# Kernel tuning notes

Hardware: AMD Instinct MI355X
Metric: run time of the kernel (lower is better)

The kernel has to match this reference:

```python
import jax, jax.numpy as jnp
import numpy as np

FEAT = 1024
ADA = 1024
INTER = 1024
RANK = 8
EPS = 1e-5


def setup_inputs() -> dict:
    key = jax.random.key(0)
    ks = jax.random.split(key, 6)
    B, T = 16, 1024
    x = jax.random.normal(ks[0], (B, T, FEAT), dtype=jnp.float32)
    ada_emb = jax.random.normal(ks[1], (B, ADA), dtype=jnp.float32)
    # learned params (fan-in scaled for numerical sanity)
    W1 = jax.random.normal(ks[2], (ADA, INTER), dtype=jnp.float32) / np.sqrt(ADA)
    b1 = jnp.zeros((INTER,), dtype=jnp.float32)
    W2 = jax.random.normal(ks[3], (INTER, FEAT * RANK * 4), dtype=jnp.float32) * (0.1 / np.sqrt(INTER))
    b2 = jnp.zeros((FEAT * RANK * 4,), dtype=jnp.float32)
    ln_g = jnp.ones((ADA,), dtype=jnp.float32)
    ln_b = jnp.zeros((ADA,), dtype=jnp.float32)
    return {"x": x, "ada_emb": ada_emb, "ln_g": ln_g, "ln_b": ln_b,
            "W1": W1, "b1": b1, "W2": W2, "b2": b2}


def _layernorm(a, g, b):
    mu = jnp.mean(a, axis=-1, keepdims=True)
    var = jnp.mean(jnp.square(a - mu), axis=-1, keepdims=True)
    return (a - mu) * jax.lax.rsqrt(var + EPS) * g + b


def reference(x, ada_emb, ln_g, ln_b, W1, b1, W2, b2):
    B, T, D = x.shape
    # hypernetwork: generate per-sample LoRA factors
    h = jax.nn.gelu(_layernorm(ada_emb, ln_g, ln_b) @ W1 + b1, approximate=False)
    w = h @ W2 + b2                                    # [B, 4*D*rank]
    a1, bb1, a2, bb2 = jnp.split(w, 4, axis=-1)
    a1 = a1.reshape(B, D, RANK)
    bb1 = bb1.reshape(B, D, RANK)
    a2 = a2.reshape(B, D, RANK)
    bb2 = bb2.reshape(B, D, RANK)
    # chained low-rank bmms, broadcast over tokens (== repeat_interleave in torch)
    y = jnp.einsum('btd,bdr->btr', x, a1)
    y = jnp.einsum('btr,bdr->btd', y, bb1)
    y = jax.nn.gelu(y, approximate=False)
    y = jnp.einsum('btd,bdr->btr', y, a2)
    y = jnp.einsum('btr,bdr->btd', y, bb2)
    return y + x
```

## Files before the change

### kernel.cpp

```cpp
#include <hip/hip_runtime.h>
#include <math.h>

typedef unsigned int u32;
typedef unsigned short u16;
typedef unsigned long long u64;

__device__ __forceinline__ u16 f2bf(float f){
  union{float f;u32 u;}v; v.f=f;
  u32 u=v.u; u += 0x7fffu + ((u>>16)&1u);
  return (u16)(u>>16);
}
__device__ __forceinline__ float gelu_exact(float z){
  return 0.5f*z*(1.f + erff(z*0.7071067811865476f));
}
__device__ __forceinline__ void ld8(const uint4* fq, int arr, int d, float* o){
  uint4 v = fq[arr*1024 + d];
  union{u32 i;float f;}c;
  c.i = v.x<<16;        o[0]=c.f;  c.i = v.x&0xffff0000u; o[1]=c.f;
  c.i = v.y<<16;        o[2]=c.f;  c.i = v.y&0xffff0000u; o[3]=c.f;
  c.i = v.z<<16;        o[4]=c.f;  c.i = v.z&0xffff0000u; o[5]=c.f;
  c.i = v.w<<16;        o[6]=c.f;  c.i = v.w&0xffff0000u; o[7]=c.f;
}

__global__ __launch_bounds__(256) void k_hyper1(
    const float* __restrict__ ada, const float* __restrict__ lng, const float* __restrict__ lnb,
    const float* __restrict__ W1, const float* __restrict__ b1, float* __restrict__ hT)
{
  __shared__ float lns[1024];
  __shared__ float red[8];
  __shared__ float cmb[256];
  const int b = blockIdx.y;
  const int tid = threadIdx.x;
  float a4[4]; float s=0.f, s2=0.f;
  #pragma unroll
  for (int i=0;i<4;i++){
    float v = ada[(size_t)b*1024 + tid + 256*i];
    a4[i]=v; s+=v; s2+=v*v;
  }
  #pragma unroll
  for (int m=32;m>=1;m>>=1){ s += __shfl_xor(s,m,64); s2 += __shfl_xor(s2,m,64); }
  if ((tid&63)==0){ red[tid>>6]=s; red[4+(tid>>6)]=s2; }
  __syncthreads();
  s  = red[0]+red[1]+red[2]+red[3];
  s2 = red[4]+red[5]+red[6]+red[7];
  const float mu = s*(1.f/1024.f);
  const float rs = rsqrtf(s2*(1.f/1024.f) - mu*mu + 1e-5f);
  #pragma unroll
  for (int i=0;i<4;i++){
    int k = tid + 256*i;
    lns[k] = (a4[i]-mu)*rs*lng[k] + lnb[k];
  }
  __syncthreads();
  const int c = tid&31;
  const int kq = tid>>5;
  const int col = (blockIdx.x<<5) + c;
  float acc = 0.f;
  #pragma unroll 8
  for (int k=kq*128; k<kq*128+128; k++)
    acc = fmaf(lns[k], W1[(size_t)k*1024 + col], acc);
  cmb[c*8 + kq] = acc;
  __syncthreads();
  if (tid < 32){
    float v = b1[(blockIdx.x<<5) + tid];
    #pragma unroll
    for (int q=0;q<8;q++) v += cmb[tid*8 + q];
    hT[(size_t)((blockIdx.x<<5) + tid)*16 + b] = gelu_exact(v);
  }
}

__global__ __launch_bounds__(256) void k_hyper2(
    const float* __restrict__ hT, const float* __restrict__ W2, const float* __restrict__ b2,
    float* __restrict__ w)
{
  __shared__ float cmb[64*65];
  const int tid = threadIdx.x;
  const int c = tid&63;
  const int kq = tid>>6;
  const int col = (blockIdx.x<<6) + c;
  const float* hbase = hT + (size_t)__builtin_amdgcn_readfirstlane(kq) * 256 * 16;
  float acc[16];
  #pragma unroll
  for (int i=0;i<16;i++) acc[i]=0.f;
  #pragma unroll 4
  for (int k=0;k<256;k++){
    float wv = W2[(size_t)(kq*256 + k)*32768 + col];
    const float* hk = hbase + k*16;
    #pragma unroll
    for (int bb=0;bb<16;bb++) acc[bb] = fmaf(hk[bb], wv, acc[bb]);
  }
  #pragma unroll
  for (int bb=0;bb<16;bb++) cmb[c*65 + kq*16 + bb] = acc[bb];
  __syncthreads();
  if (kq==0){
    float bv = b2[col];
    #pragma unroll
    for (int bb=0;bb<16;bb++)
      w[(size_t)bb*32768 + col] =
        cmb[c*65+bb] + cmb[c*65+16+bb] + cmb[c*65+32+bb] + cmb[c*65+48+bb] + bv;
  }
}

__global__ __launch_bounds__(256, 2) void k_lora(
    const float* __restrict__ x, const float* __restrict__ w, float* __restrict__ out)
{
  __shared__ __align__(16) u16 fsb[4*1024*8];
  const int b = blockIdx.y;
  const int tid = threadIdx.x;
  const float* wb = w + (size_t)b*32768;
  {
    const float4* w4 = (const float4*)wb;
    #pragma unroll 4
    for (int j=0;j<32;j++){
      const int idx4 = tid + 256*j;
      float4 v = w4[idx4];
      union{u16 h[4]; u64 u;} pk;
      pk.h[0]=f2bf(v.x); pk.h[1]=f2bf(v.y);
      pk.h[2]=f2bf(v.z); pk.h[3]=f2bf(v.w);
      *(u64*)&fsb[idx4*4] = pk.u;
    }
  }
  __syncthreads();
  const int l = tid&63;
  const int wv = tid>>6;
  const uint4* fq = (const uint4*)fsb;
  const size_t xbase = (size_t)b*1024*1024;

  #pragma unroll 1
  for (int round=0; round<4; round++){
    const int t0 = blockIdx.x*32 + wv*8 + round*2;
    const float* xr = x + xbase + (size_t)t0*1024 + l;
    float xv0[16], xv1[16];
    #pragma unroll
    for (int i=0;i<16;i++){ xv0[i]=xr[64*i]; xv1[i]=xr[1024+64*i]; }

    float y10[8], y11[8];
    #pragma unroll
    for (int r=0;r<8;r++){ y10[r]=0.f; y11[r]=0.f; }
    #pragma unroll
    for (int i=0;i<16;i++){
      float a[8]; ld8(fq, 0, l+64*i, a);
      #pragma unroll
      for (int r=0;r<8;r++){
        y10[r] = fmaf(xv0[i], a[r], y10[r]);
        y11[r] = fmaf(xv1[i], a[r], y11[r]);
      }
      if ((i&3)==3) __builtin_amdgcn_sched_barrier(0);
    }
    #pragma unroll
    for (int m=32;m>=1;m>>=1){
      #pragma unroll
      for (int r=0;r<8;r++){
        y10[r] += __shfl_xor(y10[r], m, 64);
        y11[r] += __shfl_xor(y11[r], m, 64);
      }
    }

    float y20[8], y21[8];
    #pragma unroll
    for (int r=0;r<8;r++){ y20[r]=0.f; y21[r]=0.f; }
    #pragma unroll
    for (int i=0;i<16;i++){
      float p[8]; ld8(fq, 1, l+64*i, p);
      float z0=0.f, z1=0.f;
      #pragma unroll
      for (int r=0;r<8;r++){ z0=fmaf(y10[r],p[r],z0); z1=fmaf(y11[r],p[r],z1); }
      float g0=gelu_exact(z0), g1=gelu_exact(z1);
      float q[8]; ld8(fq, 2, l+64*i, q);
      #pragma unroll
      for (int r=0;r<8;r++){ y20[r]=fmaf(g0,q[r],y20[r]); y21[r]=fmaf(g1,q[r],y21[r]); }
      if ((i&3)==3) __builtin_amdgcn_sched_barrier(0);
    }
    #pragma unroll
    for (int m=32;m>=1;m>>=1){
      #pragma unroll
      for (int r=0;r<8;r++){
        y20[r] += __shfl_xor(y20[r], m, 64);
        y21[r] += __shfl_xor(y21[r], m, 64);
      }
    }

    #pragma unroll
    for (int i=0;i<16;i++){
      float cc[8]; ld8(fq, 3, l+64*i, cc);
      float o0 = xv0[i], o1 = xv1[i];
      #pragma unroll
      for (int r=0;r<8;r++){
        o0 = fmaf(y20[r], cc[r], o0);
        o1 = fmaf(y21[r], cc[r], o1);
      }
      out[xbase + (size_t)t0*1024 + l + 64*i] = o0;
      out[xbase + (size_t)(t0+1)*1024 + l + 64*i] = o1;
      if ((i&3)==3) __builtin_amdgcn_sched_barrier(0);
    }
  }
}

extern "C" void kernel_launch(void* const* d_in, const int* in_sizes, int n_in,
                              void* d_out, int out_size, void* d_ws, size_t ws_size,
                              hipStream_t stream){
  const float* x    = (const float*)d_in[0];
  const float* ada  = (const float*)d_in[1];
  const float* lng  = (const float*)d_in[2];
  const float* lnb  = (const float*)d_in[3];
  const float* W1   = (const float*)d_in[4];
  const float* b1   = (const float*)d_in[5];
  const float* W2   = (const float*)d_in[6];
  const float* b2   = (const float*)d_in[7];
  float* out = (float*)d_out;
  float* hT  = (float*)d_ws;
  float* w   = (float*)((char*)d_ws + 65536);

  k_hyper1<<<dim3(32,16), 256, 0, stream>>>(ada, lng, lnb, W1, b1, hT);
  k_hyper2<<<dim3(512,1), 256, 0, stream>>>(hT, W2, b2, w);
  k_lora  <<<dim3(32,16), 256, 0, stream>>>(x, w, out);
}
```

Before: 305.0 us.

## Emit bf16 LoRA factors in permuted layout and vectorize x/out access

```diff
diff --git a/kernel.cpp b/kernel.cpp
--- a/kernel.cpp
+++ b/kernel.cpp
@@ -13,8 +13,8 @@
 __device__ __forceinline__ float gelu_exact(float z){
   return 0.5f*z*(1.f + erff(z*0.7071067811865476f));
 }
-__device__ __forceinline__ void ld8(const uint4* fq, int arr, int d, float* o){
-  uint4 v = fq[arr*1024 + d];
+__device__ __forceinline__ void ld8s(const uint4* fq, int slot, float* o){
+  uint4 v = fq[slot];
   union{u32 i;float f;}c;
   c.i = v.x<<16;        o[0]=c.f;  c.i = v.x&0xffff0000u; o[1]=c.f;
   c.i = v.y<<16;        o[2]=c.f;  c.i = v.y&0xffff0000u; o[3]=c.f;
@@ -70,7 +70,7 @@
 
 __global__ __launch_bounds__(256) void k_hyper2(
     const float* __restrict__ hT, const float* __restrict__ W2, const float* __restrict__ b2,
-    float* __restrict__ w)
+    u16* __restrict__ w16)
 {
   __shared__ float cmb[64*65];
   const int tid = threadIdx.x;
@@ -81,7 +81,7 @@
   float acc[16];
   #pragma unroll
   for (int i=0;i<16;i++) acc[i]=0.f;
-  #pragma unroll 4
+  #pragma unroll 8
   for (int k=0;k<256;k++){
     float wv = W2[(size_t)(kq*256 + k)*32768 + col];
     const float* hk = hbase + k*16;
@@ -93,58 +93,63 @@
   __syncthreads();
   if (kq==0){
     float bv = b2[col];
-    #pragma unroll
-    for (int bb=0;bb<16;bb++)
-      w[(size_t)bb*32768 + col] =
-        cmb[c*65+bb] + cmb[c*65+16+bb] + cmb[c*65+32+bb] + cmb[c*65+48+bb] + bv;
+    const int r   = col & 7;
+    const int d   = (col >> 3) & 1023;
+    const int arr = col >> 13;
+    const int slot = (arr<<10) + ((d&3)<<8) + (d>>2);
+    u16* wrec = w16 + ((size_t)slot<<3) + r;
+    #pragma unroll
+    for (int bb=0;bb<16;bb++){
+      float v = cmb[c*65+bb] + cmb[c*65+16+bb] + cmb[c*65+32+bb] + cmb[c*65+48+bb] + bv;
+      wrec[(size_t)bb*32768] = f2bf(v);
+    }
   }
 }
 
 __global__ __launch_bounds__(256, 2) void k_lora(
-    const float* __restrict__ x, const float* __restrict__ w, float* __restrict__ out)
+    const float* __restrict__ x, const u16* __restrict__ w16, float* __restrict__ out)
 {
   __shared__ __align__(16) u16 fsb[4*1024*8];
   const int b = blockIdx.y;
   const int tid = threadIdx.x;
-  const float* wb = w + (size_t)b*32768;
   {
-    const float4* w4 = (const float4*)wb;
+    const uint4* src = (const uint4*)(w16 + (size_t)b*32768);
+    uint4* dst = (uint4*)fsb;
     #pragma unroll 4
-    for (int j=0;j<32;j++){
-      const int idx4 = tid + 256*j;
-      float4 v = w4[idx4];
-      union{u16 h[4]; u64 u;} pk;
-      pk.h[0]=f2bf(v.x); pk.h[1]=f2bf(v.y);
-      pk.h[2]=f2bf(v.z); pk.h[3]=f2bf(v.w);
-      *(u64*)&fsb[idx4*4] = pk.u;
-    }
+    for (int j=0;j<16;j++) dst[tid + 256*j] = src[tid + 256*j];
   }
   __syncthreads();
   const int l = tid&63;
   const int wv = tid>>6;
   const uint4* fq = (const uint4*)fsb;
-  const size_t xbase = (size_t)b*1024*1024;
+  const size_t xb4 = ((size_t)b<<18);
 
   #pragma unroll 1
   for (int round=0; round<4; round++){
     const int t0 = blockIdx.x*32 + wv*8 + round*2;
-    const float* xr = x + xbase + (size_t)t0*1024 + l;
-    float xv0[16], xv1[16];
-    #pragma unroll
-    for (int i=0;i<16;i++){ xv0[i]=xr[64*i]; xv1[i]=xr[1024+64*i]; }
+    const float4* xr = (const float4*)x + xb4 + ((size_t)t0<<8) + l;
+    float4 xv0[4], xv1[4];
+    #pragma unroll
+    for (int i=0;i<4;i++){ xv0[i]=xr[64*i]; xv1[i]=xr[256+64*i]; }
 
     float y10[8], y11[8];
     #pragma unroll
     for (int r=0;r<8;r++){ y10[r]=0.f; y11[r]=0.f; }
     #pragma unroll
-    for (int i=0;i<16;i++){
-      float a[8]; ld8(fq, 0, l+64*i, a);
-      #pragma unroll
-      for (int r=0;r<8;r++){
-        y10[r] = fmaf(xv0[i], a[r], y10[r]);
-        y11[r] = fmaf(xv1[i], a[r], y11[r]);
-      }
-      if ((i&3)==3) __builtin_amdgcn_sched_barrier(0);
+    for (int i=0;i<4;i++){
+      const int sb = 64*i + l;
+      const float xc0[4] = {xv0[i].x, xv0[i].y, xv0[i].z, xv0[i].w};
+      const float xc1[4] = {xv1[i].x, xv1[i].y, xv1[i].z, xv1[i].w};
+      #pragma unroll
+      for (int cc=0;cc<4;cc++){
+        float a[8]; ld8s(fq, cc*256 + sb, a);
+        #pragma unroll
+        for (int r=0;r<8;r++){
+          y10[r] = fmaf(xc0[cc], a[r], y10[r]);
+          y11[r] = fmaf(xc1[cc], a[r], y11[r]);
+        }
+      }
+      __builtin_amdgcn_sched_barrier(0);
     }
     #pragma unroll
     for (int m=32;m>=1;m>>=1){
@@ -159,16 +164,20 @@
     #pragma unroll
     for (int r=0;r<8;r++){ y20[r]=0.f; y21[r]=0.f; }
     #pragma unroll
-    for (int i=0;i<16;i++){
-      float p[8]; ld8(fq, 1, l+64*i, p);
-      float z0=0.f, z1=0.f;
-      #pragma unroll
-      for (int r=0;r<8;r++){ z0=fmaf(y10[r],p[r],z0); z1=fmaf(y11[r],p[r],z1); }
-      float g0=gelu_exact(z0), g1=gelu_exact(z1);
-      float q[8]; ld8(fq, 2, l+64*i, q);
-      #pragma unroll
-      for (int r=0;r<8;r++){ y20[r]=fmaf(g0,q[r],y20[r]); y21[r]=fmaf(g1,q[r],y21[r]); }
-      if ((i&3)==3) __builtin_amdgcn_sched_barrier(0);
+    for (int i=0;i<4;i++){
+      const int sb = 64*i + l;
+      #pragma unroll
+      for (int cc=0;cc<4;cc++){
+        float p[8]; ld8s(fq, 1024 + cc*256 + sb, p);
+        float z0=0.f, z1=0.f;
+        #pragma unroll
+        for (int r=0;r<8;r++){ z0=fmaf(y10[r],p[r],z0); z1=fmaf(y11[r],p[r],z1); }
+        float g0=gelu_exact(z0), g1=gelu_exact(z1);
+        float q[8]; ld8s(fq, 2048 + cc*256 + sb, q);
+        #pragma unroll
+        for (int r=0;r<8;r++){ y20[r]=fmaf(g0,q[r],y20[r]); y21[r]=fmaf(g1,q[r],y21[r]); }
+        __builtin_amdgcn_sched_barrier(0);
+      }
     }
     #pragma unroll
     for (int m=32;m>=1;m>>=1){
@@ -179,18 +188,27 @@
       }
     }
 
-    #pragma unroll
-    for (int i=0;i<16;i++){
-      float cc[8]; ld8(fq, 3, l+64*i, cc);
-      float o0 = xv0[i], o1 = xv1[i];
-      #pragma unroll
-      for (int r=0;r<8;r++){
-        o0 = fmaf(y20[r], cc[r], o0);
-        o1 = fmaf(y21[r], cc[r], o1);
-      }
-      out[xbase + (size_t)t0*1024 + l + 64*i] = o0;
-      out[xbase + (size_t)(t0+1)*1024 + l + 64*i] = o1;
-      if ((i&3)==3) __builtin_amdgcn_sched_barrier(0);
+    float4* op = (float4*)out + xb4 + ((size_t)t0<<8) + l;
+    #pragma unroll
+    for (int i=0;i<4;i++){
+      const int sb = 64*i + l;
+      float4 o0 = xv0[i], o1 = xv1[i];
+      float o0c[4] = {o0.x,o0.y,o0.z,o0.w};
+      float o1c[4] = {o1.x,o1.y,o1.z,o1.w};
+      #pragma unroll
+      for (int cc=0;cc<4;cc++){
+        float ccf[8]; ld8s(fq, 3072 + cc*256 + sb, ccf);
+        #pragma unroll
+        for (int r=0;r<8;r++){
+          o0c[cc] = fmaf(y20[r], ccf[r], o0c[cc]);
+          o1c[cc] = fmaf(y21[r], ccf[r], o1c[cc]);
+        }
+      }
+      o0.x=o0c[0]; o0.y=o0c[1]; o0.z=o0c[2]; o0.w=o0c[3];
+      o1.x=o1c[0]; o1.y=o1c[1]; o1.z=o1c[2]; o1.w=o1c[3];
+      op[64*i] = o0;
+      op[256+64*i] = o1;
+      __builtin_amdgcn_sched_barrier(0);
     }
   }
 }
@@ -208,9 +226,9 @@
   const float* b2   = (const float*)d_in[7];
   float* out = (float*)d_out;
   float* hT  = (float*)d_ws;
-  float* w   = (float*)((char*)d_ws + 65536);
+  u16*   w16 = (u16*)((char*)d_ws + 65536);
 
   k_hyper1<<<dim3(32,16), 256, 0, stream>>>(ada, lng, lnb, W1, b1, hT);
-  k_hyper2<<<dim3(512,1), 256, 0, stream>>>(hT, W2, b2, w);
-  k_lora  <<<dim3(32,16), 256, 0, stream>>>(x, w, out);
-}
+  k_hyper2<<<dim3(512,1), 256, 0, stream>>>(hT, W2, b2, w16);
+  k_lora  <<<dim3(32,16), 256, 0, stream>>>(x, w16, out);
+}
```

New measurement: 296.4 us. -2.8%, faster.
